# Kernel tuning notes

Hardware: AMD Instinct MI355X
Metric: run time of the kernel (lower is better)

## Reference

```python
import jax, jax.numpy as jnp
import numpy as np

NUM_EMBEDDINGS = 1024
EMBEDDING_DIM = 256
COMMITMENT_COST = 0.25


def setup_inputs() -> dict:
    key = jax.random.key(0)
    k1, k2 = jax.random.split(key)
    z_e = jax.random.normal(k1, (64, EMBEDDING_DIM, 32, 32), dtype=jnp.float32)
    # codebook init: uniform(-1/K, 1/K), matching nn.Embedding init in the module
    emb = jax.random.uniform(k2, (NUM_EMBEDDINGS, EMBEDDING_DIM), dtype=jnp.float32,
                             minval=-1.0 / NUM_EMBEDDINGS, maxval=1.0 / NUM_EMBEDDINGS)
    return {"z_e": z_e, "emb": emb}


def reference(z_e, emb):
    B, D, H, W = z_e.shape
    K = emb.shape[0]
    z = jnp.transpose(z_e, (0, 2, 3, 1))          # [B,H,W,D]
    x = z.reshape(-1, D)                           # [N,D], N = B*H*W
    dists = (jnp.sum(x * x, axis=1, keepdims=True)
             + jnp.sum(emb * emb, axis=1)[None, :]
             - 2.0 * (x @ emb.T))
    idx = jnp.argmin(dists, axis=1)                # [N] int
    z_q = emb[idx].reshape(z.shape)                # [B,H,W,D]
    e_latent_loss = jnp.mean((jax.lax.stop_gradient(z_q) - z) ** 2)
    q_latent_loss = jnp.mean((z_q - jax.lax.stop_gradient(z)) ** 2)
    loss = q_latent_loss + COMMITMENT_COST * e_latent_loss
    # straight-through estimator
    z_q_st = z + jax.lax.stop_gradient(z_q - z)
    counts = jnp.bincount(idx, length=K).astype(z.dtype)
    avg_probs = counts / jnp.asarray(x.shape[0], z.dtype)
    perplexity = jnp.exp(-jnp.sum(avg_probs * jnp.log(avg_probs + 1e-10)))
    return jnp.transpose(z_q_st, (0, 3, 1, 2)), loss, perplexity, idx
```

## Files before the change

kernel.cpp:

```cpp
#include <hip/hip_runtime.h>
#include <hip/hip_fp16.h>
#include <stdint.h>


#define D_DIM   256
#define K_CODES 1024
#define N_ROWS  65536
#define N_ELEM  16777216
#define IDX_OFF 16777218
#define FLAG_MARGIN 1.5e-4f
#define AMB_CAP 65536
#define A_SCALE 16.0f
#define B_SCALE 4096.0f
#define INV_SCALE2 3.0517578125e-05f

typedef short short8 __attribute__((ext_vector_type(8)));
typedef _Float16 half8 __attribute__((ext_vector_type(8)));
typedef float f32x4  __attribute__((ext_vector_type(4)));

__device__ __forceinline__ unsigned int mono(float s) {
    unsigned int u = __float_as_uint(s);
    return (u & 0x80000000u) ? ~u : (u | 0x80000000u);
}
__device__ __forceinline__ float unmono(unsigned int u) {
    return __uint_as_float((u & 0x80000000u) ? (u & 0x7FFFFFFFu) : ~u);
}
__device__ __forceinline__ unsigned short f16_rne(float x) {
    return __half_as_ushort(__float2half(x));
}
__device__ __forceinline__ void gld16(const void* g, void* l) {
    __builtin_amdgcn_global_load_lds(
        (const __attribute__((address_space(1))) unsigned int*)g,
        (__attribute__((address_space(3))) unsigned int*)l, 16, 0, 0);
}

__launch_bounds__(256)
__global__ void prep_kernel(const float* __restrict__ z_e,
                            const float* __restrict__ emb,
                            unsigned short* __restrict__ A_hi,
                            float* __restrict__ xnorm,
                            float* __restrict__ enorm,
                            unsigned short* __restrict__ B_hi,
                            float* __restrict__ embT,
                            int* __restrict__ counts,
                            float* __restrict__ loss_sum,
                            int* __restrict__ amb_count) {
#pragma clang fp contract(off)
    __shared__ float T[32][257];
    __shared__ float H[32][2];
    const int tid = threadIdx.x;
    const int bid = blockIdx.x;

    if (bid < 4) {
        const int k = bid * 256 + tid;
        counts[k] = 0;
        if (bid == 0 && tid == 0) { *loss_sum = 0.f; *amb_count = 0; }
        const float* p = emb + (size_t)k * D_DIM;
        unsigned int* dstB = (unsigned int*)(B_hi + (size_t)k * D_DIM);
        float halfv[2];
        #pragma unroll
        for (int h = 0; h < 2; ++h) {
            float r[8];
            #pragma unroll
            for (int qq = 0; qq < 2; ++qq) {
                float4 ev[16];
                const float* qb = p + h * 128 + qq * 64;
                #pragma unroll
                for (int m = 0; m < 16; ++m)
                    ev[m] = *(const float4*)(qb + 4 * m);
                #pragma unroll
                for (int t = 0; t < 8; ++t) {
                    const float4 a = ev[2 * t], b = ev[2 * t + 1];
                    if (qq == 0 && t == 0) {
                        r[0] = a.x * a.x; r[1] = a.y * a.y; r[2] = a.z * a.z; r[3] = a.w * a.w;
                        r[4] = b.x * b.x; r[5] = b.y * b.y; r[6] = b.z * b.z; r[7] = b.w * b.w;
                    } else {
                        r[0] += a.x * a.x; r[1] += a.y * a.y; r[2] += a.z * a.z; r[3] += a.w * a.w;
                        r[4] += b.x * b.x; r[5] += b.y * b.y; r[6] += b.z * b.z; r[7] += b.w * b.w;
                    }
                }
                #pragma unroll
                for (int m = 0; m < 16; m += 2) {
                    const float4 a = ev[m], b = ev[m + 1];
                    unsigned int u0 = f16_rne(a.x * B_SCALE) | ((unsigned int)f16_rne(a.y * B_SCALE) << 16);
                    unsigned int u1 = f16_rne(a.z * B_SCALE) | ((unsigned int)f16_rne(a.w * B_SCALE) << 16);
                    unsigned int u2 = f16_rne(b.x * B_SCALE) | ((unsigned int)f16_rne(b.y * B_SCALE) << 16);
                    unsigned int u3 = f16_rne(b.z * B_SCALE) | ((unsigned int)f16_rne(b.w * B_SCALE) << 16);
                    *(uint4*)(dstB + (h * 64 + qq * 32 + 2 * m)) = make_uint4(u0, u1, u2, u3);
                }
                const int dbase = h * 128 + qq * 64;
                #pragma unroll
                for (int m = 0; m < 16; ++m) {
                    embT[(size_t)(dbase + 4 * m + 0) * K_CODES + k] = ev[m].x;
                    embT[(size_t)(dbase + 4 * m + 1) * K_CODES + k] = ev[m].y;
                    embT[(size_t)(dbase + 4 * m + 2) * K_CODES + k] = ev[m].z;
                    embT[(size_t)(dbase + 4 * m + 3) * K_CODES + k] = ev[m].w;
                }
            }
            halfv[h] = ((r[0] + r[1]) + (r[2] + r[3])) + ((r[4] + r[5]) + (r[6] + r[7]));
        }
        enorm[k] = halfv[0] + halfv[1];
        return;
    }

    const int bx = bid - 4;
    const int b = bx >> 5, hw0 = (bx & 31) << 5;
    const float* zb = z_e + (size_t)b * 262144 + hw0;
    #pragma unroll 4
    for (int it = 0; it < 8; ++it) {
        int flat = it * 256 + tid;
        int d = flat >> 3;
        int hw4 = (flat & 7) << 2;
        float4 v = *(const float4*)(zb + (size_t)d * 1024 + hw4);
        T[hw4 + 0][d] = v.x; T[hw4 + 1][d] = v.y;
        T[hw4 + 2][d] = v.z; T[hw4 + 3][d] = v.w;
    }
    __syncthreads();
    if (tid < 64) {
        int row = tid >> 1, h = tid & 1;
        const float* q = &T[row][h * 128];
        float r[8];
        #pragma unroll
        for (int j = 0; j < 8; ++j) { float x = q[j]; r[j] = x * x; }
        for (int i = 8; i < 128; i += 8)
            #pragma unroll
            for (int j = 0; j < 8; ++j) { float x = q[i + j]; r[j] = r[j] + x * x; }
        H[row][h] = ((r[0] + r[1]) + (r[2] + r[3])) + ((r[4] + r[5]) + (r[6] + r[7]));
    }
    __syncthreads();
    if (tid < 32) xnorm[b * 1024 + hw0 + tid] = H[tid][0] + H[tid][1];
    {
        int row = tid >> 3, seg8 = tid & 7;
        const float* src = &T[row][seg8 * 32];
        unsigned short* dst = A_hi + ((size_t)(b * 1024 + hw0 + row) * 256 + seg8 * 32);
        #pragma unroll
        for (int c = 0; c < 4; ++c) {
            unsigned int ub[4];
            #pragma unroll
            for (int p = 0; p < 4; ++p) {
                unsigned int lo = f16_rne(src[c * 8 + 2 * p] * A_SCALE);
                unsigned int hi = f16_rne(src[c * 8 + 2 * p + 1] * A_SCALE);
                ub[p] = lo | (hi << 16);
            }
            *(uint4*)(dst + c * 8) = make_uint4(ub[0], ub[1], ub[2], ub[3]);
        }
    }
}

__launch_bounds__(256, 2)
__global__ void dist2_kernel(const unsigned short* __restrict__ A_hi,
                             const unsigned short* __restrict__ B_hi,
                             const float* __restrict__ xnorm,
                             const float* __restrict__ enorm,
                             int* __restrict__ fidx,
                             int* __restrict__ amb,
                             int* __restrict__ amb_count) {
    __shared__ __align__(16) char smem[81920];
    unsigned long long* red = (unsigned long long*)(smem + 65536);

    const int tid  = threadIdx.x;
    const int lane = tid & 63, w = tid >> 6;
    const int quad = lane >> 4, l16 = lane & 15;
    const int wr = w >> 1, wc = w & 1;
    const int row0 = blockIdx.x * 128;

    const int aq    = (((lane & 3) ^ ((lane >> 3) & 3)) << 3);
    const int arsub = (w << 4) + (lane >> 2);
    const int rdoff = ((quad ^ ((l16 >> 1) & 3)) << 4);

    #pragma unroll
    for (int t = 0; t < 16; ++t) {
        const int arow = ((t & 1) << 6) + arsub;
        const int s    = t >> 1;
        gld16(A_hi + (((size_t)(row0 + arow)) << 8) + s * 32 + aq,
              smem + t * 4096 + w * 1024);
    }
    gld16(B_hi + (((size_t)(arsub)) << 8) + aq,       smem + 65536 + w * 1024);
    gld16(B_hi + (((size_t)(64 + arsub)) << 8) + aq,  smem + 65536 + 4096 + w * 1024);
    __syncthreads();

    float xnr[4][4];
    #pragma unroll
    for (int i = 0; i < 4; ++i)
        #pragma unroll
        for (int r = 0; r < 4; ++r)
            xnr[i][r] = xnorm[row0 + wr * 64 + i * 16 + quad * 4 + r];

    const float INF = __uint_as_float(0x7F800000u);
    float m1[4][4], m2[4][4];
    unsigned int ix[4][4];
    #pragma unroll
    for (int i = 0; i < 4; ++i)
        #pragma unroll
        for (int r = 0; r < 4; ++r) { m1[i][r] = INF; m2[i][r] = INF; ix[i][r] = 0u; }

    int cur = 0;
    for (int cb = 0; cb < 8; ++cb) {
        f32x4 acc[4][4];
        #pragma unroll
        for (int i = 0; i < 4; ++i)
            #pragma unroll
            for (int j = 0; j < 4; ++j) acc[i][j] = (f32x4){0.f, 0.f, 0.f, 0.f};

        for (int s = 0; s < 8; ++s) {
            const int nstep = cb * 8 + s + 1;
            if (nstep < 64) {
                const int ncb = nstep >> 3, ns = nstep & 7;
                char* nb = smem + 65536 + ((cur ^ 1) << 13);
                gld16(B_hi + (((size_t)(ncb * 128 + arsub)) << 8) + ns * 32 + aq,
                      nb + w * 1024);
                gld16(B_hi + (((size_t)(ncb * 128 + 64 + arsub)) << 8) + ns * 32 + aq,
                      nb + 4096 + w * 1024);
            }
            const char* bb = smem + 65536 + (cur << 13);
            half8 af[4], bf[4];
            #pragma unroll
            for (int i = 0; i < 4; ++i)
                af[i] = *(const half8*)(smem + s * 8192 + (wr * 64 + i * 16 + l16) * 64 + rdoff);
            #pragma unroll
            for (int j = 0; j < 4; ++j)
                bf[j] = *(const half8*)(bb + (wc * 64 + j * 16 + l16) * 64 + rdoff);
            __builtin_amdgcn_s_setprio(1);
            #pragma unroll
            for (int i = 0; i < 4; ++i)
                #pragma unroll
                for (int j = 0; j < 4; ++j)
                    acc[i][j] = __builtin_amdgcn_mfma_f32_16x16x32_f16(af[i], bf[j], acc[i][j], 0, 0, 0);
            __builtin_amdgcn_s_setprio(0);
            __syncthreads();
            cur ^= 1;
        }

        float enj[4];
        #pragma unroll
        for (int j = 0; j < 4; ++j) enj[j] = enorm[cb * 128 + wc * 64 + j * 16 + l16];
        #pragma unroll
        for (int i = 0; i < 4; ++i) {
            #pragma unroll
            for (int r = 0; r < 4; ++r) {
                const float xn = xnr[i][r];
                float a = m1[i][r], b = m2[i][r];
                unsigned int id = ix[i][r];
                #pragma unroll
                for (int j = 0; j < 4; ++j) {
                    const unsigned int n = cb * 128 + wc * 64 + j * 16 + l16;
                    float sc = fmaf(acc[i][j][r], -INV_SCALE2, xn + enj[j]);
                    bool c = sc < a;
                    b = fminf(b, fmaxf(a, sc));
                    a = fminf(a, sc);
                    id = c ? n : id;
                }
                m1[i][r] = a; m2[i][r] = b; ix[i][r] = id;
            }
        }
    }

    #pragma unroll
    for (int i = 0; i < 4; ++i) {
        #pragma unroll
        for (int r = 0; r < 4; ++r) {
            unsigned long long a1 = ((unsigned long long)mono(m1[i][r]) << 32) | ix[i][r];
            unsigned long long a2 = ((unsigned long long)mono(m2[i][r]) << 32) | 0xFFFFFFFFull;
            #pragma unroll
            for (int m = 1; m < 16; m <<= 1) {
                unsigned long long q1 = __shfl_xor(a1, m, 16);
                unsigned long long q2 = __shfl_xor(a2, m, 16);
                if (q1 < a1) { a2 = (a1 < q2) ? a1 : q2; a1 = q1; }
                else         { a2 = (a2 < q1) ? a2 : q1; }
            }
            if (l16 == 0) {
                int rowl = wr * 64 + i * 16 + quad * 4 + r;
                red[(rowl * 2 + wc) * 2 + 0] = a1;
                red[(rowl * 2 + wc) * 2 + 1] = a2;
            }
        }
    }
    __syncthreads();
    if (tid < 128) {
        unsigned long long a1 = red[(tid * 2 + 0) * 2 + 0];
        unsigned long long a2 = red[(tid * 2 + 0) * 2 + 1];
        unsigned long long b1 = red[(tid * 2 + 1) * 2 + 0];
        unsigned long long b2 = red[(tid * 2 + 1) * 2 + 1];
        if (b1 < a1) { a2 = (a1 < b2) ? a1 : b2; a1 = b1; }
        else         { a2 = (a2 < b1) ? a2 : b1; }
        const int row = row0 + tid;
        fidx[row] = (int)(a1 & 0xFFFFFFFFull);
        float s1 = unmono((unsigned int)(a1 >> 32));
        float s2 = unmono((unsigned int)(a2 >> 32));
        if (s2 - s1 <= FLAG_MARGIN) {
            int slot = atomicAdd(amb_count, 1);
            if (slot < AMB_CAP) amb[slot] = row;
        }
    }
}

__launch_bounds__(256)
__global__ void rescue4_kernel(const float* __restrict__ z_e,
                               const float* __restrict__ embT,
                               const float* __restrict__ xnorm,
                               const float* __restrict__ enorm,
                               const int* __restrict__ amb,
                               const int* __restrict__ amb_count,
                               int* __restrict__ fidx) {
    __shared__ float xs[4][256];
    __shared__ int rows[4];
    __shared__ unsigned long long pm[4][257];
    const int tid = threadIdx.x;
    int cnt = *amb_count;
    if (cnt > AMB_CAP) cnt = AMB_CAP;
    if (cnt <= 0) return;
    const int ngroups = (cnt + 3) >> 2;
    for (int g = blockIdx.x; g < ngroups; g += gridDim.x) {
        if (tid < 4) {
            int e = g * 4 + tid;
            rows[tid] = amb[e < cnt ? e : (cnt - 1)];
        }
        __syncthreads();
        {
            const int j = tid >> 6, d0 = (tid & 63) * 4;
            const int row = rows[j];
            const int b = row >> 10, hw = row & 1023;
            const float* zp = z_e + (size_t)b * 262144 + hw;
            #pragma unroll
            for (int i = 0; i < 4; ++i)
                xs[j][d0 + i] = zp[(size_t)(d0 + i) * 1024];
        }
        __syncthreads();

        double acc[4][4];
        #pragma unroll
        for (int c = 0; c < 4; ++c)
            #pragma unroll
            for (int j = 0; j < 4; ++j) acc[c][j] = 0.0;

        const float* ep = embT + 4 * tid;
        for (int d0 = 0; d0 < D_DIM; d0 += 8) {
            float4 ev[8];
            #pragma unroll
            for (int u = 0; u < 8; ++u)
                ev[u] = *(const float4*)(ep + (size_t)(d0 + u) * K_CODES);
            #pragma unroll
            for (int u = 0; u < 8; ++u) {
                const int d = d0 + u;
                double e0 = (double)ev[u].x, e1 = (double)ev[u].y;
                double e2 = (double)ev[u].z, e3 = (double)ev[u].w;
                double x0 = (double)xs[0][d], x1 = (double)xs[1][d];
                double x2 = (double)xs[2][d], x3 = (double)xs[3][d];
                acc[0][0] += x0 * e0; acc[0][1] += x1 * e0; acc[0][2] += x2 * e0; acc[0][3] += x3 * e0;
                acc[1][0] += x0 * e1; acc[1][1] += x1 * e1; acc[1][2] += x2 * e1; acc[1][3] += x3 * e1;
                acc[2][0] += x0 * e2; acc[2][1] += x1 * e2; acc[2][2] += x2 * e2; acc[2][3] += x3 * e2;
                acc[3][0] += x0 * e3; acc[3][1] += x1 * e3; acc[3][2] += x2 * e3; acc[3][3] += x3 * e3;
            }
        }

        float xnr[4];
        #pragma unroll
        for (int j = 0; j < 4; ++j) xnr[j] = xnorm[rows[j]];

        unsigned long long mm[4] = {~0ull, ~0ull, ~0ull, ~0ull};
        #pragma unroll
        for (int c = 0; c < 4; ++c) {
            const int k = 4 * tid + c;
            const float en = enorm[k];
            #pragma unroll
            for (int j = 0; j < 4; ++j) {
                float dv = (float)acc[c][j];
                float t = xnr[j] + en;
                float s = t - 2.f * dv;
                unsigned long long p = ((unsigned long long)mono(s) << 32) | (unsigned int)k;
                if (p < mm[j]) mm[j] = p;
            }
        }
        #pragma unroll
        for (int j = 0; j < 4; ++j) pm[j][tid] = mm[j];
        __syncthreads();
        for (int s = 128; s > 0; s >>= 1) {
            if (tid < s) {
                #pragma unroll
                for (int j = 0; j < 4; ++j)
                    if (pm[j][tid + s] < pm[j][tid]) pm[j][tid] = pm[j][tid + s];
            }
            __syncthreads();
        }
        if (tid < 4) fidx[rows[tid]] = (int)(pm[tid][0] & 0xFFFFFFFFull);
        __syncthreads();
    }
}

__global__ void epilogue_kernel(const float* __restrict__ z_e,
                                const float* __restrict__ emb,
                                const int* __restrict__ fidx,
                                float* __restrict__ out,
                                int* __restrict__ counts,
                                float* __restrict__ loss_sum) {
    __shared__ int   kb[64];
    __shared__ float rs[256];
    const int tid = threadIdx.x;
    const int rcb = blockIdx.x;
    const int b   = rcb >> 4;
    const int hw0 = (rcb & 15) << 6;

    if (tid < 64) {
        int k = fidx[rcb * 64 + tid];
        kb[tid] = k;
        out[(size_t)IDX_OFF + (size_t)rcb * 64 + tid] = (float)k;
        atomicAdd(&counts[k], 1);
    }
    __syncthreads();

    const int j4 = (tid & 15) << 2;
    const int dq = tid >> 4;
    const float* e0 = emb + (size_t)kb[j4 + 0] * D_DIM;
    const float* e1 = emb + (size_t)kb[j4 + 1] * D_DIM;
    const float* e2 = emb + (size_t)kb[j4 + 2] * D_DIM;
    const float* e3 = emb + (size_t)kb[j4 + 3] * D_DIM;
    const size_t base = (size_t)b * 262144 + hw0 + j4;
    float ls = 0.f;
    #pragma unroll 4
    for (int d = dq; d < D_DIM; d += 16) {
        size_t off = base + ((size_t)d << 10);
        float4 x = *(const float4*)(z_e + off);
        float4 q;
        q.x = e0[d]; q.y = e1[d]; q.z = e2[d]; q.w = e3[d];
        *(float4*)(out + off) = q;
        float d0 = q.x - x.x, d1 = q.y - x.y, d2 = q.z - x.z, d3 = q.w - x.w;
        ls += d0 * d0; ls += d1 * d1; ls += d2 * d2; ls += d3 * d3;
    }
    rs[tid] = ls;
    __syncthreads();
    for (int s = 128; s > 0; s >>= 1) {
        if (tid < s) rs[tid] += rs[tid + s];
        __syncthreads();
    }
    if (tid == 0) atomicAdd(loss_sum, rs[0]);
}

__global__ void finalize_kernel(const int* __restrict__ counts,
                                const float* __restrict__ loss_sum,
                                float* __restrict__ out) {
    __shared__ float rs[256];
    const int tid = threadIdx.x;
    float s = 0.f;
    for (int k = tid; k < K_CODES; k += 256) {
        float p = (float)counts[k] / 65536.0f;
        s += p * logf(p + 1e-10f);
    }
    rs[tid] = s;
    __syncthreads();
    for (int st = 128; st > 0; st >>= 1) {
        if (tid < st) rs[tid] += rs[tid + st];
        __syncthreads();
    }
    if (tid == 0) {
        out[N_ELEM]     = loss_sum[0] * 1.25f / 16777216.0f;
        out[N_ELEM + 1] = expf(-rs[0]);
    }
}

extern "C" void kernel_launch(void* const* d_in, const int* in_sizes, int n_in,
                              void* d_out, int out_size, void* d_ws, size_t ws_size,
                              hipStream_t stream) {
    const float* z_e = (const float*)d_in[0];
    const float* emb = (const float*)d_in[1];
    float* out = (float*)d_out;
    char*  ws  = (char*)d_ws;

    unsigned short* A_hi = (unsigned short*)d_out;

    float*          enorm    = (float*)ws;
    float*          xnorm    = (float*)(ws + 4096);
    int*            fidx     = (int*)(ws + 266240);
    int*            counts   = (int*)(ws + 528384);
    float*          loss_sum = (float*)(ws + 532480);
    int*            amb_cnt  = (int*)(ws + 532484);
    int*            amb      = (int*)(ws + 532488);
    unsigned short* B_hi     = (unsigned short*)(ws + 794752);
    float*          embT     = (float*)(ws + 1319040);

    prep_kernel<<<2052, 256, 0, stream>>>(z_e, emb, A_hi, xnorm, enorm, B_hi, embT,
                                          counts, loss_sum, amb_cnt);
    dist2_kernel<<<512, 256, 0, stream>>>(A_hi, B_hi, xnorm, enorm, fidx, amb, amb_cnt);
    rescue4_kernel<<<1024, 256, 0, stream>>>(z_e, embT, xnorm, enorm, amb, amb_cnt, fidx);
    epilogue_kernel<<<N_ROWS / 64, 256, 0, stream>>>(z_e, emb, fidx, out, counts, loss_sum);
    finalize_kernel<<<1, 256, 0, stream>>>(counts, loss_sum, out);
}
```

Measured before the change: 281.8 us.

## Register-prefetch codebook tiles two steps ahead and fold finalize into epilogue

The distance GEMM now loads B codebook tiles from global into registers two steps ahead and writes them to LDS after the MFMAs, replacing async global_load_lds double-buffering. The goal is to hide global latency behind compute with explicit scheduling barriers and a single s_barrier per step. The finalize kernel is also merged into the epilogue through a last-block-done atomic counter, saving one launch. The trade-offs are higher register pressure under launch bounds of 2 blocks per SM and an extra atomic and fence in every epilogue block.

```diff
diff --git a/kernel.cpp b/kernel.cpp
--- a/kernel.cpp
+++ b/kernel.cpp
@@ -44,17 +44,18 @@
                             float* __restrict__ embT,
                             int* __restrict__ counts,
                             float* __restrict__ loss_sum,
-                            int* __restrict__ amb_count) {
+                            int* __restrict__ amb_count,
+                            int* __restrict__ done) {
 #pragma clang fp contract(off)
     __shared__ float T[32][257];
     __shared__ float H[32][2];
+    const int bid = blockIdx.x;
     const int tid = threadIdx.x;
-    const int bid = blockIdx.x;
 
     if (bid < 4) {
         const int k = bid * 256 + tid;
         counts[k] = 0;
-        if (bid == 0 && tid == 0) { *loss_sum = 0.f; *amb_count = 0; }
+        if (bid == 0 && tid == 0) { *loss_sum = 0.f; *amb_count = 0; *done = 0; }
         const float* p = emb + (size_t)k * D_DIM;
         unsigned int* dstB = (unsigned int*)(B_hi + (size_t)k * D_DIM);
         float halfv[2];
@@ -63,8 +64,8 @@
             float r[8];
             #pragma unroll
             for (int qq = 0; qq < 2; ++qq) {
+                const float* qb = p + h * 128 + qq * 64;
                 float4 ev[16];
-                const float* qb = p + h * 128 + qq * 64;
                 #pragma unroll
                 for (int m = 0; m < 16; ++m)
                     ev[m] = *(const float4*)(qb + 4 * m);
@@ -147,6 +148,38 @@
     }
 }
 
+#define DSTEP(T, CUR, W0, W1, I0, I1)                                                   \
+  {                                                                                     \
+    const int t_ = (T);                                                                 \
+    if (t_ + 2 < 64) {                                                                  \
+      const int nc_ = (t_ + 2) >> 3, ns_ = (t_ + 2) & 7;                                \
+      I0 = *(const uint4*)(B_hi + (((size_t)(nc_ * 128 + arsub)) << 8) + ns_ * 32 + aq);      \
+      I1 = *(const uint4*)(B_hi + (((size_t)(nc_ * 128 + 64 + arsub)) << 8) + ns_ * 32 + aq); \
+    }                                                                                   \
+    __builtin_amdgcn_sched_barrier(0);                                                  \
+    const char* bb_ = smem + 65536 + ((CUR) << 13);                                     \
+    const int sv_ = t_ & 7;                                                             \
+    half8 af[4], bf[4];                                                                 \
+    _Pragma("unroll") for (int i = 0; i < 4; ++i)                                       \
+      af[i] = *(const half8*)(smem + sv_ * 8192 + (wr * 64 + i * 16 + l16) * 64 + rdoff); \
+    _Pragma("unroll") for (int j = 0; j < 4; ++j)                                       \
+      bf[j] = *(const half8*)(bb_ + (wc * 64 + j * 16 + l16) * 64 + rdoff);             \
+    __builtin_amdgcn_s_setprio(1);                                                      \
+    _Pragma("unroll") for (int i = 0; i < 4; ++i)                                       \
+      _Pragma("unroll") for (int j = 0; j < 4; ++j)                                     \
+        acc[i][j] = __builtin_amdgcn_mfma_f32_16x16x32_f16(af[i], bf[j], acc[i][j], 0, 0, 0); \
+    __builtin_amdgcn_s_setprio(0);                                                      \
+    __builtin_amdgcn_sched_barrier(0);                                                  \
+    if (t_ + 1 < 64) {                                                                  \
+      char* nb_ = smem + 65536 + ((1 ^ (CUR)) << 13) + w * 1024 + (lane << 4);          \
+      *(uint4*)nb_ = W0;                                                                \
+      *(uint4*)(nb_ + 4096) = W1;                                                       \
+    }                                                                                   \
+    asm volatile("s_waitcnt lgkmcnt(0)" ::: "memory");                                  \
+    __builtin_amdgcn_s_barrier();                                                       \
+    __builtin_amdgcn_sched_barrier(0);                                                  \
+  }
+
 __launch_bounds__(256, 2)
 __global__ void dist2_kernel(const unsigned short* __restrict__ A_hi,
                              const unsigned short* __restrict__ B_hi,
@@ -159,9 +192,9 @@
     unsigned long long* red = (unsigned long long*)(smem + 65536);
 
     const int tid  = threadIdx.x;
-    const int lane = tid & 63, w = tid >> 6;
-    const int quad = lane >> 4, l16 = lane & 15;
-    const int wr = w >> 1, wc = w & 1;
+    const int w = tid >> 6, lane = tid & 63;
+    const int l16 = lane & 15, quad = lane >> 4;
+    const int wc = w & 1, wr = w >> 1;
     const int row0 = blockIdx.x * 128;
 
     const int aq    = (((lane & 3) ^ ((lane >> 3) & 3)) << 3);
@@ -175,9 +208,19 @@
         gld16(A_hi + (((size_t)(row0 + arow)) << 8) + s * 32 + aq,
               smem + t * 4096 + w * 1024);
     }
-    gld16(B_hi + (((size_t)(arsub)) << 8) + aq,       smem + 65536 + w * 1024);
-    gld16(B_hi + (((size_t)(64 + arsub)) << 8) + aq,  smem + 65536 + 4096 + w * 1024);
-    __syncthreads();
+    uint4 p0, p1, q0, q1;
+    p0 = *(const uint4*)(B_hi + (((size_t)(arsub)) << 8) + aq);
+    p1 = *(const uint4*)(B_hi + (((size_t)(64 + arsub)) << 8) + aq);
+    q0 = *(const uint4*)(B_hi + (((size_t)(arsub)) << 8) + 32 + aq);
+    q1 = *(const uint4*)(B_hi + (((size_t)(64 + arsub)) << 8) + 32 + aq);
+    {
+        char* d0 = smem + 65536 + w * 1024 + (lane << 4);
+        *(uint4*)d0 = p0;
+        *(uint4*)(d0 + 4096) = p1;
+    }
+    asm volatile("s_waitcnt lgkmcnt(0)" ::: "memory");
+    __builtin_amdgcn_s_barrier();
+    __builtin_amdgcn_sched_barrier(0);
 
     float xnr[4][4];
     #pragma unroll
@@ -194,7 +237,6 @@
         #pragma unroll
         for (int r = 0; r < 4; ++r) { m1[i][r] = INF; m2[i][r] = INF; ix[i][r] = 0u; }
 
-    int cur = 0;
     for (int cb = 0; cb < 8; ++cb) {
         f32x4 acc[4][4];
         #pragma unroll
@@ -202,33 +244,10 @@
             #pragma unroll
             for (int j = 0; j < 4; ++j) acc[i][j] = (f32x4){0.f, 0.f, 0.f, 0.f};
 
-        for (int s = 0; s < 8; ++s) {
-            const int nstep = cb * 8 + s + 1;
-            if (nstep < 64) {
-                const int ncb = nstep >> 3, ns = nstep & 7;
-                char* nb = smem + 65536 + ((cur ^ 1) << 13);
-                gld16(B_hi + (((size_t)(ncb * 128 + arsub)) << 8) + ns * 32 + aq,
-                      nb + w * 1024);
-                gld16(B_hi + (((size_t)(ncb * 128 + 64 + arsub)) << 8) + ns * 32 + aq,
-                      nb + 4096 + w * 1024);
-            }
-            const char* bb = smem + 65536 + (cur << 13);
-            half8 af[4], bf[4];
-            #pragma unroll
-            for (int i = 0; i < 4; ++i)
-                af[i] = *(const half8*)(smem + s * 8192 + (wr * 64 + i * 16 + l16) * 64 + rdoff);
-            #pragma unroll
-            for (int j = 0; j < 4; ++j)
-                bf[j] = *(const half8*)(bb + (wc * 64 + j * 16 + l16) * 64 + rdoff);
-            __builtin_amdgcn_s_setprio(1);
-            #pragma unroll
-            for (int i = 0; i < 4; ++i)
-                #pragma unroll
-                for (int j = 0; j < 4; ++j)
-                    acc[i][j] = __builtin_amdgcn_mfma_f32_16x16x32_f16(af[i], bf[j], acc[i][j], 0, 0, 0);
-            __builtin_amdgcn_s_setprio(0);
-            __syncthreads();
-            cur ^= 1;
+        #pragma unroll
+        for (int sh = 0; sh < 4; ++sh) {
+            DSTEP(cb * 8 + 2 * sh,     0, q0, q1, p0, p1);
+            DSTEP(cb * 8 + 2 * sh + 1, 1, p0, p1, q0, q1);
         }
 
         float enj[4];
@@ -263,10 +282,10 @@
             unsigned long long a2 = ((unsigned long long)mono(m2[i][r]) << 32) | 0xFFFFFFFFull;
             #pragma unroll
             for (int m = 1; m < 16; m <<= 1) {
-                unsigned long long q1 = __shfl_xor(a1, m, 16);
-                unsigned long long q2 = __shfl_xor(a2, m, 16);
-                if (q1 < a1) { a2 = (a1 < q2) ? a1 : q2; a1 = q1; }
-                else         { a2 = (a2 < q1) ? a2 : q1; }
+                unsigned long long u1 = __shfl_xor(a1, m, 16);
+                unsigned long long u2 = __shfl_xor(a2, m, 16);
+                if (u1 < a1) { a2 = (a1 < u2) ? a1 : u2; a1 = u1; }
+                else         { a2 = (a2 < u1) ? a2 : u1; }
             }
             if (l16 == 0) {
                 int rowl = wr * 64 + i * 16 + quad * 4 + r;
@@ -392,9 +411,11 @@
                                 const int* __restrict__ fidx,
                                 float* __restrict__ out,
                                 int* __restrict__ counts,
-                                float* __restrict__ loss_sum) {
+                                float* __restrict__ loss_sum,
+                                int* __restrict__ done) {
     __shared__ int   kb[64];
     __shared__ float rs[256];
+    __shared__ int   lastFlag;
     const int tid = threadIdx.x;
     const int rcb = blockIdx.x;
     const int b   = rcb >> 4;
@@ -433,27 +454,29 @@
         __syncthreads();
     }
     if (tid == 0) atomicAdd(loss_sum, rs[0]);
-}
-
-__global__ void finalize_kernel(const int* __restrict__ counts,
-                                const float* __restrict__ loss_sum,
-                                float* __restrict__ out) {
-    __shared__ float rs[256];
-    const int tid = threadIdx.x;
-    float s = 0.f;
-    for (int k = tid; k < K_CODES; k += 256) {
-        float p = (float)counts[k] / 65536.0f;
-        s += p * logf(p + 1e-10f);
-    }
-    rs[tid] = s;
+
+    __threadfence();
+    if (tid == 0) lastFlag = (atomicAdd(done, 1) == (int)gridDim.x - 1);
     __syncthreads();
-    for (int st = 128; st > 0; st >>= 1) {
-        if (tid < st) rs[tid] += rs[tid + st];
+    if (lastFlag) {
+        __threadfence();
+        float s = 0.f;
+        for (int k = tid; k < K_CODES; k += 256) {
+            int c = atomicAdd(&counts[k], 0);
+            float p = (float)c / 65536.0f;
+            s += p * logf(p + 1e-10f);
+        }
+        rs[tid] = s;
         __syncthreads();
-    }
-    if (tid == 0) {
-        out[N_ELEM]     = loss_sum[0] * 1.25f / 16777216.0f;
-        out[N_ELEM + 1] = expf(-rs[0]);
+        for (int st = 128; st > 0; st >>= 1) {
+            if (tid < st) rs[tid] += rs[tid + st];
+            __syncthreads();
+        }
+        if (tid == 0) {
+            float L = atomicAdd(loss_sum, 0.f);
+            out[N_ELEM]     = L * 1.25f / 16777216.0f;
+            out[N_ELEM + 1] = expf(-rs[0]);
+        }
     }
 }
 
@@ -474,13 +497,13 @@
     float*          loss_sum = (float*)(ws + 532480);
     int*            amb_cnt  = (int*)(ws + 532484);
     int*            amb      = (int*)(ws + 532488);
+    int*            done     = (int*)(ws + 794632);
     unsigned short* B_hi     = (unsigned short*)(ws + 794752);
     float*          embT     = (float*)(ws + 1319040);
 
     prep_kernel<<<2052, 256, 0, stream>>>(z_e, emb, A_hi, xnorm, enorm, B_hi, embT,
-                                          counts, loss_sum, amb_cnt);
+                                          counts, loss_sum, amb_cnt, done);
     dist2_kernel<<<512, 256, 0, stream>>>(A_hi, B_hi, xnorm, enorm, fidx, amb, amb_cnt);
     rescue4_kernel<<<1024, 256, 0, stream>>>(z_e, embT, xnorm, enorm, amb, amb_cnt, fidx);
-    epilogue_kernel<<<N_ROWS / 64, 256, 0, stream>>>(z_e, emb, fidx, out, counts, loss_sum);
-    finalize_kernel<<<1, 256, 0, stream>>>(counts, loss_sum, out);
-}
+    epilogue_kernel<<<N_ROWS / 64, 256, 0, stream>>>(z_e, emb, fidx, out, counts, loss_sum, done);
+}
```

After: 423.2 us. 50.2% more time.
